# Optimization experiments

Measured on AMD Instinct MI355X. Metric: run time of the kernel, lower is better.

Reference implementation:

```python
import jax, jax.numpy as jnp
import numpy as np

TIME_STEPS = 20
PREDICT_STEPS = 20
REC_MAX_ENC = 2.0 ** (1.0 / TIME_STEPS)
REC_MAX_DEC = 2.0 ** (1.0 / PREDICT_STEPS)
BATCH = 4096
HIDDEN = 1024
IN = 2


def _indrnn_layer(x, W, u, b):
    """One IndRNN layer, seq-first. x: (T,B,I) -> (T,B,H).
    h_t = relu(W x_t + b + u * h_{t-1}), u is elementwise (diagonal) recurrent weight."""
    pre = jnp.einsum('tbi,hi->tbh', x, W) + b  # one big GEMM over all timesteps

    def step(h, p):
        h = jax.nn.relu(p + u * h)
        return h, h

    h0 = jnp.zeros(pre.shape[1:], pre.dtype)
    _, ys = jax.lax.scan(step, h0, pre)
    return ys


def setup_inputs() -> dict:
    key = jax.random.key(0)
    ks = jax.random.split(key, 16)
    f32 = jnp.float32

    def lin_w(k, out_d, in_d):
        return (jax.random.normal(k, (out_d, in_d), f32) / np.sqrt(in_d)).astype(f32)

    def rec_u(k, h, umax):
        return jax.random.uniform(k, (h,), f32, -umax, umax)

    inp = {
        'x': jax.random.normal(ks[0], (TIME_STEPS, BATCH, IN), f32),
        # encoder layers (2)
        'enc_w0': lin_w(ks[1], HIDDEN, IN),
        'enc_u0': rec_u(ks[2], HIDDEN, REC_MAX_ENC),
        'enc_b0': jnp.zeros((HIDDEN,), f32),
        'enc_w1': lin_w(ks[3], HIDDEN, HIDDEN),
        'enc_u1': rec_u(ks[4], HIDDEN, REC_MAX_ENC),
        'enc_b1': jnp.zeros((HIDDEN,), f32),
        # decoder layers (2)
        'dec_w0': lin_w(ks[5], HIDDEN, HIDDEN),
        'dec_u0': rec_u(ks[6], HIDDEN, REC_MAX_DEC),
        'dec_b0': jnp.zeros((HIDDEN,), f32),
        'dec_w1': lin_w(ks[7], HIDDEN, HIDDEN),
        'dec_u1': rec_u(ks[8], HIDDEN, REC_MAX_DEC),
        'dec_b1': jnp.zeros((HIDDEN,), f32),
        # output head: Linear(hidden, 2)
        'out_w': lin_w(ks[9], 2, HIDDEN),
        'out_b': jnp.zeros((2,), f32),
    }
    return inp


def reference(x, enc_w0, enc_u0, enc_b0, enc_w1, enc_u1, enc_b1,
              dec_w0, dec_u0, dec_b0, dec_w1, dec_u1, dec_b1,
              out_w, out_b):
    # encoder: 2-layer IndRNN, seq-first
    y = _indrnn_layer(x, enc_w0, enc_u0, enc_b0)          # (T,B,H)
    y = _indrnn_layer(y, enc_w1, enc_u1, enc_b1)          # (T,B,H)
    # y[:, -1] -> (T,H); .expand(PREDICT_STEPS, -1, H) prepends a dim -> (P,T,H)
    last = y[:, -1]                                        # (T,H)
    temp = jnp.broadcast_to(last, (PREDICT_STEPS,) + last.shape)  # (P,T,H)
    # decoder: 2-layer IndRNN over seq dim P with batch T
    out = _indrnn_layer(temp, dec_w0, dec_u0, dec_b0)
    out = _indrnn_layer(out, dec_w1, dec_u1, dec_b1)       # (P,T,H)
    # out[:, 0] -> (P,H); Linear head -> (P,2)
    predict = out[:, 0] @ out_w.T + out_b
    return predict
```

## Files before the change

kernel.cpp:

```cpp
#include <hip/hip_runtime.h>


#define HID 1024
#define TSTEPS 20

__device__ __forceinline__ float wred(float v) {
#pragma unroll
    for (int off = 32; off > 0; off >>= 1) v += __shfl_down(v, off, 64);
    return v;
}

__global__ __launch_bounds__(256) void k_enc(
    const float* __restrict__ x, const float* __restrict__ w0,
    const float* __restrict__ b0, const float* __restrict__ w1,
    const float* __restrict__ b1, float* __restrict__ last0) {
    __shared__ float v0s[HID];
    const float x0 = x[(0 * 4096 + 4095) * 2 + 0];
    const float x1 = x[(0 * 4096 + 4095) * 2 + 1];
    for (int i = threadIdx.x; i < HID; i += 256)
        v0s[i] = fmaxf(fmaf(w0[2 * i], x0, fmaf(w0[2 * i + 1], x1, b0[i])), 0.f);
    __syncthreads();
    const int wave = threadIdx.x >> 6, lane = threadIdx.x & 63;
    const int h = blockIdx.x * 4 + wave;
    const float4* wrow = (const float4*)(w1 + h * HID);
    float s = 0.f;
#pragma unroll
    for (int k = 0; k < 4; ++k) {
        float4 wv = wrow[lane * 4 + k];
        int ib = lane * 16 + k * 4;
        s = fmaf(wv.x, v0s[ib + 0], s);
        s = fmaf(wv.y, v0s[ib + 1], s);
        s = fmaf(wv.z, v0s[ib + 2], s);
        s = fmaf(wv.w, v0s[ib + 3], s);
    }
    s = wred(s);
    if (lane == 0) last0[h] = fmaxf(s + b1[h], 0.f);
}

__global__ __launch_bounds__(256) void k_dec0(
    const float* __restrict__ last0, const float* __restrict__ w0,
    const float* __restrict__ u0, const float* __restrict__ b0,
    float* __restrict__ G) {
    __shared__ float l0[HID];
    for (int i = threadIdx.x; i < HID; i += 256) l0[i] = last0[i];
    __syncthreads();
    const int wave = threadIdx.x >> 6, lane = threadIdx.x & 63;
    const int h = blockIdx.x * 4 + wave;
    const float4* wrow = (const float4*)(w0 + h * HID);
    float s = 0.f;
#pragma unroll
    for (int k = 0; k < 4; ++k) {
        float4 wv = wrow[lane * 4 + k];
        int ib = lane * 16 + k * 4;
        s = fmaf(wv.x, l0[ib + 0], s);
        s = fmaf(wv.y, l0[ib + 1], s);
        s = fmaf(wv.z, l0[ib + 2], s);
        s = fmaf(wv.w, l0[ib + 3], s);
    }
    s = wred(s);
    if (lane == 0) {
        const float p = s + b0[h], uu = u0[h];
        float g = 0.f;
#pragma unroll
        for (int t = 0; t < TSTEPS; ++t) {
            g = fmaxf(fmaf(uu, g, p), 0.f);
            G[t * HID + h] = g;
        }
    }
}

__global__ __launch_bounds__(256) void k_dec1(
    const float* __restrict__ G, const float* __restrict__ w1,
    const float* __restrict__ u1, const float* __restrict__ b1,
    float* __restrict__ H1) {
    const int wave = threadIdx.x >> 6, lane = threadIdx.x & 63;
    const int h = blockIdx.x * 4 + wave;
    const float4* wrow = (const float4*)(w1 + h * HID);
    float4 w[4];
#pragma unroll
    for (int k = 0; k < 4; ++k) w[k] = wrow[lane * 4 + k];
    const float uu = u1[h], bb = b1[h];
    float hh = 0.f;
    for (int t = 0; t < TSTEPS; ++t) {
        const float4* gt = (const float4*)(G + t * HID);
        float s = 0.f;
#pragma unroll
        for (int k = 0; k < 4; ++k) {
            float4 gv = gt[lane * 4 + k];
            s = fmaf(w[k].x, gv.x, s);
            s = fmaf(w[k].y, gv.y, s);
            s = fmaf(w[k].z, gv.z, s);
            s = fmaf(w[k].w, gv.w, s);
        }
        s = wred(s);
        hh = fmaxf(fmaf(uu, hh, s + bb), 0.f);
        if (lane == 0) H1[t * HID + h] = hh;
    }
}

__global__ __launch_bounds__(256) void k_out(
    const float* __restrict__ H1, const float* __restrict__ ow,
    const float* __restrict__ ob, float* __restrict__ out) {
    const int t = blockIdx.x, tid = threadIdx.x;
    const float4* hv = (const float4*)(H1 + t * HID);
    const float4* wa = (const float4*)(ow);
    const float4* wb = (const float4*)(ow + HID);
    float4 h4 = hv[tid], a = wa[tid], b = wb[tid];
    float s0 = h4.x * a.x + h4.y * a.y + h4.z * a.z + h4.w * a.w;
    float s1 = h4.x * b.x + h4.y * b.y + h4.z * b.z + h4.w * b.w;
    s0 = wred(s0);
    s1 = wred(s1);
    __shared__ float p[8];
    const int wave = tid >> 6, lane = tid & 63;
    if (lane == 0) {
        p[wave * 2 + 0] = s0;
        p[wave * 2 + 1] = s1;
    }
    __syncthreads();
    if (tid == 0) out[t * 2 + 0] = p[0] + p[2] + p[4] + p[6] + ob[0];
    if (tid == 1) out[t * 2 + 1] = p[1] + p[3] + p[5] + p[7] + ob[1];
}

extern "C" void kernel_launch(void* const* d_in, const int* in_sizes, int n_in,
                              void* d_out, int out_size, void* d_ws, size_t ws_size,
                              hipStream_t stream) {
    const float* x      = (const float*)d_in[0];
    const float* enc_w0 = (const float*)d_in[1];
    const float* enc_b0 = (const float*)d_in[3];
    const float* enc_w1 = (const float*)d_in[4];
    const float* enc_b1 = (const float*)d_in[6];
    const float* dec_w0 = (const float*)d_in[7];
    const float* dec_u0 = (const float*)d_in[8];
    const float* dec_b0 = (const float*)d_in[9];
    const float* dec_w1 = (const float*)d_in[10];
    const float* dec_u1 = (const float*)d_in[11];
    const float* dec_b1 = (const float*)d_in[12];
    const float* out_w  = (const float*)d_in[13];
    const float* out_b  = (const float*)d_in[14];
    float* out = (float*)d_out;

    float* ws    = (float*)d_ws;
    float* last0 = ws;
    float* G     = ws + HID;
    float* H1    = ws + HID + TSTEPS * HID;

    k_enc<<<256, 256, 0, stream>>>(x, enc_w0, enc_b0, enc_w1, enc_b1, last0);
    k_dec0<<<256, 256, 0, stream>>>(last0, dec_w0, dec_u0, dec_b0, G);
    k_dec1<<<256, 256, 0, stream>>>(G, dec_w1, dec_u1, dec_b1, H1);
    k_out<<<20, 256, 0, stream>>>(H1, out_w, out_b, out);
}
```

Before: 109.9 us.

## Fuse encoder, decoder and output head into one persistent kernel with grid barriers

Replaces the four separate kernel launches with a single persistent kernel of 512 blocks that synchronises its stages through an atomic-counter grid barrier, plus a tiny kernel that resets the counter. Each block now computes two hidden rows with all 256 threads cooperating per row. In the second decoder layer, timesteps are split across the four waves instead of looping serially in one wave. The aim is to remove inter-kernel launch gaps and make better use of the GPU, at the cost of spin-wait barriers that assume all 512 blocks are resident at once.

```diff
diff --git a/kernel.cpp b/kernel.cpp
--- a/kernel.cpp
+++ b/kernel.cpp
@@ -3,122 +3,146 @@
 
 #define HID 1024
 #define TSTEPS 20
+#define NBLK 512
 
-__device__ __forceinline__ float wred(float v) {
+__device__ __forceinline__ float wred64(float v) {
 #pragma unroll
     for (int off = 32; off > 0; off >>= 1) v += __shfl_down(v, off, 64);
     return v;
 }
 
-__global__ __launch_bounds__(256) void k_enc(
-    const float* __restrict__ x, const float* __restrict__ w0,
-    const float* __restrict__ b0, const float* __restrict__ w1,
-    const float* __restrict__ b1, float* __restrict__ last0) {
-    __shared__ float v0s[HID];
-    const float x0 = x[(0 * 4096 + 4095) * 2 + 0];
-    const float x1 = x[(0 * 4096 + 4095) * 2 + 1];
-    for (int i = threadIdx.x; i < HID; i += 256)
-        v0s[i] = fmaxf(fmaf(w0[2 * i], x0, fmaf(w0[2 * i + 1], x1, b0[i])), 0.f);
+__device__ __forceinline__ void gbar(int* bar, int k) {
     __syncthreads();
-    const int wave = threadIdx.x >> 6, lane = threadIdx.x & 63;
-    const int h = blockIdx.x * 4 + wave;
-    const float4* wrow = (const float4*)(w1 + h * HID);
-    float s = 0.f;
-#pragma unroll
-    for (int k = 0; k < 4; ++k) {
-        float4 wv = wrow[lane * 4 + k];
-        int ib = lane * 16 + k * 4;
-        s = fmaf(wv.x, v0s[ib + 0], s);
-        s = fmaf(wv.y, v0s[ib + 1], s);
-        s = fmaf(wv.z, v0s[ib + 2], s);
-        s = fmaf(wv.w, v0s[ib + 3], s);
+    if (threadIdx.x == 0) {
+        __threadfence();
+        __hip_atomic_fetch_add(bar, 1, __ATOMIC_RELEASE, __HIP_MEMORY_SCOPE_AGENT);
+        while (__hip_atomic_load(bar, __ATOMIC_ACQUIRE, __HIP_MEMORY_SCOPE_AGENT) < NBLK * k)
+            __builtin_amdgcn_s_sleep(1);
+        __threadfence();
     }
-    s = wred(s);
-    if (lane == 0) last0[h] = fmaxf(s + b1[h], 0.f);
+    __syncthreads();
 }
 
-__global__ __launch_bounds__(256) void k_dec0(
-    const float* __restrict__ last0, const float* __restrict__ w0,
-    const float* __restrict__ u0, const float* __restrict__ b0,
-    float* __restrict__ G) {
-    __shared__ float l0[HID];
-    for (int i = threadIdx.x; i < HID; i += 256) l0[i] = last0[i];
-    __syncthreads();
-    const int wave = threadIdx.x >> 6, lane = threadIdx.x & 63;
-    const int h = blockIdx.x * 4 + wave;
-    const float4* wrow = (const float4*)(w0 + h * HID);
-    float s = 0.f;
+__global__ void k_init(int* bar) { *bar = 0; }
+
+__global__ __launch_bounds__(256, 2) void k_fused(
+    const float* __restrict__ x,
+    const float* __restrict__ ew0, const float* __restrict__ eb0,
+    const float* __restrict__ ew1, const float* __restrict__ eb1,
+    const float* __restrict__ dw0, const float* __restrict__ du0,
+    const float* __restrict__ db0,
+    const float* __restrict__ dw1, const float* __restrict__ du1,
+    const float* __restrict__ db1,
+    const float* __restrict__ ow, const float* __restrict__ ob,
+    float* __restrict__ out,
+    float* __restrict__ last0, float* __restrict__ G, float* __restrict__ H1,
+    int* __restrict__ bar)
+{
+    const int tid = threadIdx.x, b = blockIdx.x;
+    const int wave = tid >> 6, lane = tid & 63;
+    __shared__ float v0s[HID];
+    __shared__ float red[8];
+    __shared__ float ps[2];
+    __shared__ float qs[2][TSTEPS];
+
+    {
+        const float x0 = x[8190], x1 = x[8191];
 #pragma unroll
-    for (int k = 0; k < 4; ++k) {
-        float4 wv = wrow[lane * 4 + k];
-        int ib = lane * 16 + k * 4;
-        s = fmaf(wv.x, l0[ib + 0], s);
-        s = fmaf(wv.y, l0[ib + 1], s);
-        s = fmaf(wv.z, l0[ib + 2], s);
-        s = fmaf(wv.w, l0[ib + 3], s);
-    }
-    s = wred(s);
-    if (lane == 0) {
-        const float p = s + b0[h], uu = u0[h];
-        float g = 0.f;
+        for (int i = tid; i < HID; i += 256) {
+            float2 w2 = ((const float2*)ew0)[i];
+            v0s[i] = fmaxf(fmaf(w2.x, x0, fmaf(w2.y, x1, eb0[i])), 0.f);
+        }
+        __syncthreads();
 #pragma unroll
-        for (int t = 0; t < TSTEPS; ++t) {
-            g = fmaxf(fmaf(uu, g, p), 0.f);
-            G[t * HID + h] = g;
+        for (int rr = 0; rr < 2; ++rr) {
+            const int r = b + rr * NBLK;
+            float4 wv = ((const float4*)(ew1 + r * HID))[tid];
+            float4 vv = ((const float4*)v0s)[tid];
+            float s = wv.x * vv.x + wv.y * vv.y + wv.z * vv.z + wv.w * vv.w;
+            s = wred64(s);
+            if (lane == 0) red[wave] = s;
+            __syncthreads();
+            if (tid == 0)
+                last0[r] = fmaxf(red[0] + red[1] + red[2] + red[3] + eb1[r], 0.f);
+            __syncthreads();
         }
     }
-}
+    gbar(bar, 1);
 
-__global__ __launch_bounds__(256) void k_dec1(
-    const float* __restrict__ G, const float* __restrict__ w1,
-    const float* __restrict__ u1, const float* __restrict__ b1,
-    float* __restrict__ H1) {
-    const int wave = threadIdx.x >> 6, lane = threadIdx.x & 63;
-    const int h = blockIdx.x * 4 + wave;
-    const float4* wrow = (const float4*)(w1 + h * HID);
-    float4 w[4];
+    {
+        float4 l4 = ((const float4*)last0)[tid];
 #pragma unroll
-    for (int k = 0; k < 4; ++k) w[k] = wrow[lane * 4 + k];
-    const float uu = u1[h], bb = b1[h];
-    float hh = 0.f;
-    for (int t = 0; t < TSTEPS; ++t) {
-        const float4* gt = (const float4*)(G + t * HID);
-        float s = 0.f;
+        for (int rr = 0; rr < 2; ++rr) {
+            const int r = b + rr * NBLK;
+            float4 wv = ((const float4*)(dw0 + r * HID))[tid];
+            float s = wv.x * l4.x + wv.y * l4.y + wv.z * l4.z + wv.w * l4.w;
+            s = wred64(s);
+            if (lane == 0) red[wave] = s;
+            __syncthreads();
+            if (tid == 0) ps[rr] = red[0] + red[1] + red[2] + red[3] + db0[r];
+            __syncthreads();
+        }
+        if (tid < 2) {
+            const int r = b + tid * NBLK;
+            float p = ps[tid], uu = du0[r], g = 0.f;
 #pragma unroll
-        for (int k = 0; k < 4; ++k) {
-            float4 gv = gt[lane * 4 + k];
-            s = fmaf(w[k].x, gv.x, s);
-            s = fmaf(w[k].y, gv.y, s);
-            s = fmaf(w[k].z, gv.z, s);
-            s = fmaf(w[k].w, gv.w, s);
+            for (int t = 0; t < TSTEPS; ++t) {
+                g = fmaxf(fmaf(uu, g, p), 0.f);
+                G[t * HID + r] = g;
+            }
         }
-        s = wred(s);
-        hh = fmaxf(fmaf(uu, hh, s + bb), 0.f);
-        if (lane == 0) H1[t * HID + h] = hh;
     }
-}
+    gbar(bar, 2);
 
-__global__ __launch_bounds__(256) void k_out(
-    const float* __restrict__ H1, const float* __restrict__ ow,
-    const float* __restrict__ ob, float* __restrict__ out) {
-    const int t = blockIdx.x, tid = threadIdx.x;
-    const float4* hv = (const float4*)(H1 + t * HID);
-    const float4* wa = (const float4*)(ow);
-    const float4* wb = (const float4*)(ow + HID);
-    float4 h4 = hv[tid], a = wa[tid], b = wb[tid];
-    float s0 = h4.x * a.x + h4.y * a.y + h4.z * a.z + h4.w * a.w;
-    float s1 = h4.x * b.x + h4.y * b.y + h4.z * b.z + h4.w * b.w;
-    s0 = wred(s0);
-    s1 = wred(s1);
-    __shared__ float p[8];
-    const int wave = tid >> 6, lane = tid & 63;
-    if (lane == 0) {
-        p[wave * 2 + 0] = s0;
-        p[wave * 2 + 1] = s1;
+    {
+#pragma unroll
+        for (int rr = 0; rr < 2; ++rr) {
+            const int r = b + rr * NBLK;
+            const float4* wrow = (const float4*)(dw1 + r * HID);
+            float4 w0v = wrow[lane * 4 + 0], w1v = wrow[lane * 4 + 1];
+            float4 w2v = wrow[lane * 4 + 2], w3v = wrow[lane * 4 + 3];
+            for (int t = wave; t < TSTEPS; t += 4) {
+                const float4* gt = (const float4*)(G + t * HID);
+                float4 g0 = gt[lane * 4 + 0], g1 = gt[lane * 4 + 1];
+                float4 g2 = gt[lane * 4 + 2], g3 = gt[lane * 4 + 3];
+                float s = w0v.x * g0.x + w0v.y * g0.y + w0v.z * g0.z + w0v.w * g0.w;
+                s = fmaf(w1v.x, g1.x, s); s = fmaf(w1v.y, g1.y, s);
+                s = fmaf(w1v.z, g1.z, s); s = fmaf(w1v.w, g1.w, s);
+                s = fmaf(w2v.x, g2.x, s); s = fmaf(w2v.y, g2.y, s);
+                s = fmaf(w2v.z, g2.z, s); s = fmaf(w2v.w, g2.w, s);
+                s = fmaf(w3v.x, g3.x, s); s = fmaf(w3v.y, g3.y, s);
+                s = fmaf(w3v.z, g3.z, s); s = fmaf(w3v.w, g3.w, s);
+                s = wred64(s);
+                if (lane == 0) qs[rr][t] = s;
+            }
+        }
+        __syncthreads();
+        if (tid < 2) {
+            const int r = b + tid * NBLK;
+            float uu = du1[r], bb = db1[r], hh = 0.f;
+#pragma unroll
+            for (int t = 0; t < TSTEPS; ++t) {
+                hh = fmaxf(fmaf(uu, hh, qs[tid][t] + bb), 0.f);
+                H1[t * HID + r] = hh;
+            }
+        }
     }
-    __syncthreads();
-    if (tid == 0) out[t * 2 + 0] = p[0] + p[2] + p[4] + p[6] + ob[0];
-    if (tid == 1) out[t * 2 + 1] = p[1] + p[3] + p[5] + p[7] + ob[1];
+    gbar(bar, 3);
+
+    if (b < TSTEPS) {
+        const int t = b;
+        float4 h4 = ((const float4*)(H1 + t * HID))[tid];
+        float4 a4 = ((const float4*)ow)[tid];
+        float4 b4 = ((const float4*)(ow + HID))[tid];
+        float s0 = h4.x * a4.x + h4.y * a4.y + h4.z * a4.z + h4.w * a4.w;
+        float s1 = h4.x * b4.x + h4.y * b4.y + h4.z * b4.z + h4.w * b4.w;
+        s0 = wred64(s0);
+        s1 = wred64(s1);
+        if (lane == 0) { red[wave] = s0; red[4 + wave] = s1; }
+        __syncthreads();
+        if (tid == 0) out[2 * t + 0] = red[0] + red[1] + red[2] + red[3] + ob[0];
+        if (tid == 1) out[2 * t + 1] = red[4] + red[5] + red[6] + red[7] + ob[1];
+    }
 }
 
 extern "C" void kernel_launch(void* const* d_in, const int* in_sizes, int n_in,
@@ -143,9 +167,11 @@
     float* last0 = ws;
     float* G     = ws + HID;
     float* H1    = ws + HID + TSTEPS * HID;
+    int*   bar   = (int*)(ws + 64 * 1024);
 
-    k_enc<<<256, 256, 0, stream>>>(x, enc_w0, enc_b0, enc_w1, enc_b1, last0);
-    k_dec0<<<256, 256, 0, stream>>>(last0, dec_w0, dec_u0, dec_b0, G);
-    k_dec1<<<256, 256, 0, stream>>>(G, dec_w1, dec_u1, dec_b1, H1);
-    k_out<<<20, 256, 0, stream>>>(H1, out_w, out_b, out);
+    k_init<<<1, 1, 0, stream>>>(bar);
+    k_fused<<<NBLK, 256, 0, stream>>>(
+        x, enc_w0, enc_b0, enc_w1, enc_b1,
+        dec_w0, dec_u0, dec_b0, dec_w1, dec_u1, dec_b1,
+        out_w, out_b, out, last0, G, H1, bar);
 }
```

After: 265.1 us. +141.3%, slower.

## Fuse output head into decoder layer-1 kernel via atomics, two rows per wave

Applied to the files above, without the earlier changes.

Removes the separate output-head kernel by having each wave in the decoder layer-1 kernel compute its rows' contribution to the 2-wide linear head. It reduces per block in shared memory and accumulates into the output with atomicAdd, which the encoder kernel seeds with the bias. Each wave now handles two hidden rows, so only 128 blocks are launched and each G load is reused twice. Weight and vector loads are also switched to lane-contiguous float4 access. The cost is atomic contention on 40 outputs and less parallelism in the recurrent kernel.

```diff
diff --git a/kernel.cpp b/kernel.cpp
--- a/kernel.cpp
+++ b/kernel.cpp
@@ -4,121 +4,122 @@
 #define HID 1024
 #define TSTEPS 20
 
-__device__ __forceinline__ float wred(float v) {
+__device__ __forceinline__ float wred64(float v) {
 #pragma unroll
     for (int off = 32; off > 0; off >>= 1) v += __shfl_down(v, off, 64);
     return v;
 }
 
 __global__ __launch_bounds__(256) void k_enc(
-    const float* __restrict__ x, const float* __restrict__ w0,
-    const float* __restrict__ b0, const float* __restrict__ w1,
-    const float* __restrict__ b1, float* __restrict__ last0) {
+    const float* __restrict__ x, const float* __restrict__ ew0,
+    const float* __restrict__ eb0, const float* __restrict__ ew1,
+    const float* __restrict__ eb1, const float* __restrict__ ob,
+    float* __restrict__ last0, float* __restrict__ out) {
+    const int tid = threadIdx.x, wave = tid >> 6, lane = tid & 63;
     __shared__ float v0s[HID];
-    const float x0 = x[(0 * 4096 + 4095) * 2 + 0];
-    const float x1 = x[(0 * 4096 + 4095) * 2 + 1];
-    for (int i = threadIdx.x; i < HID; i += 256)
-        v0s[i] = fmaxf(fmaf(w0[2 * i], x0, fmaf(w0[2 * i + 1], x1, b0[i])), 0.f);
+    __shared__ float red[4];
+
+    if (blockIdx.x == 0 && tid < 2 * TSTEPS) out[tid] = ob[tid & 1];
+
+    const float x0 = x[8190], x1 = x[8191];
+#pragma unroll
+    for (int i = tid; i < HID / 2; i += 256) {
+        float4 w4 = ((const float4*)ew0)[i];
+        float2 e2 = ((const float2*)eb0)[i];
+        v0s[2 * i + 0] = fmaxf(fmaf(w4.x, x0, fmaf(w4.y, x1, e2.x)), 0.f);
+        v0s[2 * i + 1] = fmaxf(fmaf(w4.z, x0, fmaf(w4.w, x1, e2.y)), 0.f);
+    }
     __syncthreads();
-    const int wave = threadIdx.x >> 6, lane = threadIdx.x & 63;
-    const int h = blockIdx.x * 4 + wave;
-    const float4* wrow = (const float4*)(w1 + h * HID);
+
+    const int r = blockIdx.x * 4 + wave;
+    const float4* wrow = (const float4*)(ew1 + r * HID);
+    const float4* v4 = (const float4*)v0s;
     float s = 0.f;
 #pragma unroll
     for (int k = 0; k < 4; ++k) {
-        float4 wv = wrow[lane * 4 + k];
-        int ib = lane * 16 + k * 4;
-        s = fmaf(wv.x, v0s[ib + 0], s);
-        s = fmaf(wv.y, v0s[ib + 1], s);
-        s = fmaf(wv.z, v0s[ib + 2], s);
-        s = fmaf(wv.w, v0s[ib + 3], s);
+        float4 w = wrow[k * 64 + lane], v = v4[k * 64 + lane];
+        s = fmaf(w.x, v.x, s); s = fmaf(w.y, v.y, s);
+        s = fmaf(w.z, v.z, s); s = fmaf(w.w, v.w, s);
     }
-    s = wred(s);
-    if (lane == 0) last0[h] = fmaxf(s + b1[h], 0.f);
+    s = wred64(s);
+    if (lane == 0) last0[r] = fmaxf(s + eb1[r], 0.f);
 }
 
 __global__ __launch_bounds__(256) void k_dec0(
-    const float* __restrict__ last0, const float* __restrict__ w0,
-    const float* __restrict__ u0, const float* __restrict__ b0,
+    const float* __restrict__ last0, const float* __restrict__ dw0,
+    const float* __restrict__ du0, const float* __restrict__ db0,
     float* __restrict__ G) {
+    const int tid = threadIdx.x, wave = tid >> 6, lane = tid & 63;
     __shared__ float l0[HID];
-    for (int i = threadIdx.x; i < HID; i += 256) l0[i] = last0[i];
+    ((float4*)l0)[tid] = ((const float4*)last0)[tid];
     __syncthreads();
-    const int wave = threadIdx.x >> 6, lane = threadIdx.x & 63;
-    const int h = blockIdx.x * 4 + wave;
-    const float4* wrow = (const float4*)(w0 + h * HID);
+
+    const int r = blockIdx.x * 4 + wave;
+    const float4* wrow = (const float4*)(dw0 + r * HID);
+    const float4* v4 = (const float4*)l0;
     float s = 0.f;
 #pragma unroll
     for (int k = 0; k < 4; ++k) {
-        float4 wv = wrow[lane * 4 + k];
-        int ib = lane * 16 + k * 4;
-        s = fmaf(wv.x, l0[ib + 0], s);
-        s = fmaf(wv.y, l0[ib + 1], s);
-        s = fmaf(wv.z, l0[ib + 2], s);
-        s = fmaf(wv.w, l0[ib + 3], s);
+        float4 w = wrow[k * 64 + lane], v = v4[k * 64 + lane];
+        s = fmaf(w.x, v.x, s); s = fmaf(w.y, v.y, s);
+        s = fmaf(w.z, v.z, s); s = fmaf(w.w, v.w, s);
     }
-    s = wred(s);
+    s = wred64(s);
     if (lane == 0) {
-        const float p = s + b0[h], uu = u0[h];
+        const float p = s + db0[r], uu = du0[r];
         float g = 0.f;
 #pragma unroll
         for (int t = 0; t < TSTEPS; ++t) {
             g = fmaxf(fmaf(uu, g, p), 0.f);
-            G[t * HID + h] = g;
+            G[t * HID + r] = g;
         }
     }
 }
 
-__global__ __launch_bounds__(256) void k_dec1(
-    const float* __restrict__ G, const float* __restrict__ w1,
-    const float* __restrict__ u1, const float* __restrict__ b1,
-    float* __restrict__ H1) {
-    const int wave = threadIdx.x >> 6, lane = threadIdx.x & 63;
-    const int h = blockIdx.x * 4 + wave;
-    const float4* wrow = (const float4*)(w1 + h * HID);
-    float4 w[4];
+__global__ __launch_bounds__(256) void k_dec1_out(
+    const float* __restrict__ G, const float* __restrict__ dw1,
+    const float* __restrict__ du1, const float* __restrict__ db1,
+    const float* __restrict__ ow, float* __restrict__ out) {
+    const int tid = threadIdx.x, wave = tid >> 6, lane = tid & 63;
+    const int rA = blockIdx.x * 8 + wave * 2, rB = rA + 1;
+    __shared__ float sh[4][TSTEPS][2];
+
+    const float4* wrA = (const float4*)(dw1 + rA * HID);
+    const float4* wrB = (const float4*)(dw1 + rB * HID);
+    float4 wa[4], wb[4];
 #pragma unroll
-    for (int k = 0; k < 4; ++k) w[k] = wrow[lane * 4 + k];
-    const float uu = u1[h], bb = b1[h];
-    float hh = 0.f;
+    for (int k = 0; k < 4; ++k) { wa[k] = wrA[k * 64 + lane]; wb[k] = wrB[k * 64 + lane]; }
+
+    const float uA = du1[rA], bA = db1[rA], o0A = ow[rA], o1A = ow[HID + rA];
+    const float uB = du1[rB], bB = db1[rB], o0B = ow[rB], o1B = ow[HID + rB];
+    float hA = 0.f, hB = 0.f;
+
     for (int t = 0; t < TSTEPS; ++t) {
         const float4* gt = (const float4*)(G + t * HID);
-        float s = 0.f;
+        float sA = 0.f, sB = 0.f;
 #pragma unroll
         for (int k = 0; k < 4; ++k) {
-            float4 gv = gt[lane * 4 + k];
-            s = fmaf(w[k].x, gv.x, s);
-            s = fmaf(w[k].y, gv.y, s);
-            s = fmaf(w[k].z, gv.z, s);
-            s = fmaf(w[k].w, gv.w, s);
+            float4 g = gt[k * 64 + lane];
+            sA = fmaf(wa[k].x, g.x, sA); sA = fmaf(wa[k].y, g.y, sA);
+            sA = fmaf(wa[k].z, g.z, sA); sA = fmaf(wa[k].w, g.w, sA);
+            sB = fmaf(wb[k].x, g.x, sB); sB = fmaf(wb[k].y, g.y, sB);
+            sB = fmaf(wb[k].z, g.z, sB); sB = fmaf(wb[k].w, g.w, sB);
         }
-        s = wred(s);
-        hh = fmaxf(fmaf(uu, hh, s + bb), 0.f);
-        if (lane == 0) H1[t * HID + h] = hh;
-    }
-}
-
-__global__ __launch_bounds__(256) void k_out(
-    const float* __restrict__ H1, const float* __restrict__ ow,
-    const float* __restrict__ ob, float* __restrict__ out) {
-    const int t = blockIdx.x, tid = threadIdx.x;
-    const float4* hv = (const float4*)(H1 + t * HID);
-    const float4* wa = (const float4*)(ow);
-    const float4* wb = (const float4*)(ow + HID);
-    float4 h4 = hv[tid], a = wa[tid], b = wb[tid];
-    float s0 = h4.x * a.x + h4.y * a.y + h4.z * a.z + h4.w * a.w;
-    float s1 = h4.x * b.x + h4.y * b.y + h4.z * b.z + h4.w * b.w;
-    s0 = wred(s0);
-    s1 = wred(s1);
-    __shared__ float p[8];
-    const int wave = tid >> 6, lane = tid & 63;
-    if (lane == 0) {
-        p[wave * 2 + 0] = s0;
-        p[wave * 2 + 1] = s1;
+        sA = wred64(sA);
+        sB = wred64(sB);
+        if (lane == 0) {
+            hA = fmaxf(fmaf(uA, hA, sA + bA), 0.f);
+            hB = fmaxf(fmaf(uB, hB, sB + bB), 0.f);
+            sh[wave][t][0] = fmaf(o0A, hA, o0B * hB);
+            sh[wave][t][1] = fmaf(o1A, hA, o1B * hB);
+        }
     }
     __syncthreads();
-    if (tid == 0) out[t * 2 + 0] = p[0] + p[2] + p[4] + p[6] + ob[0];
-    if (tid == 1) out[t * 2 + 1] = p[1] + p[3] + p[5] + p[7] + ob[1];
+    if (tid < 2 * TSTEPS) {
+        const int t = tid >> 1, j = tid & 1;
+        float v = sh[0][t][j] + sh[1][t][j] + sh[2][t][j] + sh[3][t][j];
+        atomicAdd(&out[t * 2 + j], v);
+    }
 }
 
 extern "C" void kernel_launch(void* const* d_in, const int* in_sizes, int n_in,
@@ -142,10 +143,9 @@
     float* ws    = (float*)d_ws;
     float* last0 = ws;
     float* G     = ws + HID;
-    float* H1    = ws + HID + TSTEPS * HID;
 
-    k_enc<<<256, 256, 0, stream>>>(x, enc_w0, enc_b0, enc_w1, enc_b1, last0);
+    k_enc<<<256, 256, 0, stream>>>(x, enc_w0, enc_b0, enc_w1, enc_b1,
+                                   out_b, last0, out);
     k_dec0<<<256, 256, 0, stream>>>(last0, dec_w0, dec_u0, dec_b0, G);
-    k_dec1<<<256, 256, 0, stream>>>(G, dec_w1, dec_u1, dec_b1, H1);
-    k_out<<<20, 256, 0, stream>>>(H1, out_w, out_b, out);
+    k_dec1_out<<<128, 256, 0, stream>>>(G, dec_w1, dec_u1, dec_b1, out_w, out);
 }
```

Result: no change. 109.7 us (-0.1%).
